# Kernel optimization log

Hardware: AMD Instinct MI355X
Metric: run time of the kernel (lower is better)

## Reference

```python
import jax, jax.numpy as jnp
import numpy as np

D_MODEL = 1024
HEADS = 16
D_K = D_MODEL // HEADS
LN_EPS = 1e-6  # flax nn.LayerNorm default
NEG_INF = -1000000000.0


def _layernorm(x, scale, bias):
    mu = jnp.mean(x, axis=-1, keepdims=True)
    var = jnp.var(x, axis=-1, keepdims=True)
    return (x - mu) * jax.lax.rsqrt(var + LN_EPS) * scale + bias


def setup_inputs() -> dict:
    key = jax.random.key(0)
    ks = jax.random.split(key, 8)
    bs, sq, skv = 4, 2048, 2048
    init = 1.0 / np.sqrt(D_MODEL)  # ~lecun_normal scale for Dense kernels
    return {
        "kv": jax.random.normal(ks[0], (bs, skv, D_MODEL), jnp.float32),
        "q": jax.random.normal(ks[1], (bs, sq, D_MODEL), jnp.float32),
        "mask": jax.random.randint(ks[2], (bs, sq, skv), 0, 2, jnp.int32),
        "Wq": jax.random.normal(ks[3], (D_MODEL, D_MODEL), jnp.float32) * init,
        "bq": jnp.zeros((D_MODEL,), jnp.float32),
        "Wk": jax.random.normal(ks[4], (D_MODEL, D_MODEL), jnp.float32) * init,
        "bk": jnp.zeros((D_MODEL,), jnp.float32),
        "Wv": jax.random.normal(ks[5], (D_MODEL, D_MODEL), jnp.float32) * init,
        "bv": jnp.zeros((D_MODEL,), jnp.float32),
        "qn_scale": jnp.ones((D_MODEL,), jnp.float32),
        "qn_bias": jnp.zeros((D_MODEL,), jnp.float32),
        "kn_scale": jnp.ones((D_MODEL,), jnp.float32),
        "kn_bias": jnp.zeros((D_MODEL,), jnp.float32),
        "vn_scale": jnp.ones((D_MODEL,), jnp.float32),
        "vn_bias": jnp.zeros((D_MODEL,), jnp.float32),
        "Wo": jax.random.normal(ks[6], (D_MODEL, D_MODEL), jnp.float32) * init,
        "bo": jnp.zeros((D_MODEL,), jnp.float32),
    }


def reference(kv, q, mask, Wq, bq, Wk, bk, Wv, bv,
              qn_scale, qn_bias, kn_scale, kn_bias, vn_scale, vn_bias,
              Wo, bo):
    bs = q.shape[0]
    # Dense projections + per-feature LayerNorm on Q/K/V
    query = _layernorm(q @ Wq + bq, qn_scale, qn_bias)
    key = _layernorm(kv @ Wk + bk, kn_scale, kn_bias)
    value = _layernorm(kv @ Wv + bv, vn_scale, vn_bias)
    # [b, s, h, d] -> [b, h, s, d]
    query = query.reshape(bs, -1, HEADS, D_K).transpose(0, 2, 1, 3)
    key = key.reshape(bs, -1, HEADS, D_K).transpose(0, 2, 1, 3)
    value = value.reshape(bs, -1, HEADS, D_K).transpose(0, 2, 1, 3)
    # scores: [b, h, q, k]
    scores = jnp.einsum('bhqd,bhkd->bhqk', query, key) / jnp.sqrt(jnp.asarray(D_K, query.dtype))
    m = mask[:, None, :, :]  # expand_dims(mask, axis=1)
    scores = jnp.where(m == 0, NEG_INF, scores)
    probs = jax.nn.softmax(scores, axis=-1)
    out = jnp.einsum('bhqk,bhkd->bhqd', probs, value)
    out = out.transpose(0, 2, 1, 3).reshape(bs, -1, D_MODEL)
    return out @ Wo + bo
```

## Files before the change

kernel.cpp:

```cpp
#include <hip/hip_runtime.h>
#include <hip/hip_bf16.h>

#define SEQ   2048
#define BS    4
#define DM    1024
#define NH    16
#define ROWS  (BS*SEQ)

using s16x8 = __attribute__((ext_vector_type(8))) short;
using f32x4 = __attribute__((ext_vector_type(4))) float;

#define MFMA16(a,b,c) __builtin_amdgcn_mfma_f32_16x16x32_bf16(a,b,c,0,0,0)

__device__ __forceinline__ short f2bf(float f){
  union { float f; unsigned u; } v; v.f = f;
  unsigned r = (v.u + 0x7FFFu + ((v.u >> 16) & 1u)) >> 16;
  return (short)r;
}

__device__ __forceinline__ float bf2f(short s){
  union { unsigned u; float f; } v; v.u = ((unsigned)(unsigned short)s) << 16;
  return v.f;
}

__device__ __forceinline__ float bpermf(float v, int srcLane){
  union { float f; int i; } u; u.f = v;
  u.i = __builtin_amdgcn_ds_bpermute(srcLane * 4, u.i);
  return u.f;
}

__device__ __forceinline__ void gload_lds16(const void* g, void* l){
  __builtin_amdgcn_global_load_lds(
    (const __attribute__((address_space(1))) unsigned int*)g,
    (__attribute__((address_space(3))) unsigned int*)l, 16, 0, 0);
}

__global__ __launch_bounds__(256) void pack_mask(const int* __restrict__ mask,
                                                 unsigned* __restrict__ bits){
  int t = blockIdx.x * 256 + threadIdx.x;
  unsigned long long b = __ballot(mask[t] != 0);
  int lane = threadIdx.x & 63;
  if (lane == 0)       bits[t >> 5] = (unsigned)b;
  else if (lane == 32) bits[t >> 5] = (unsigned)(b >> 32);
}

__global__ __launch_bounds__(256) void conv_bf16(const float* __restrict__ in,
                                                 short* __restrict__ out){
  int t = blockIdx.x * 256 + threadIdx.x;
  float4 v = ((const float4*)in)[t];
  short4 o;
  o.x = f2bf(v.x); o.y = f2bf(v.y); o.z = f2bf(v.z); o.w = f2bf(v.w);
  ((short4*)out)[t] = o;
}

__global__ __launch_bounds__(256) void transpose_w(const float* __restrict__ W,
                                                   short* __restrict__ Wt){
  __shared__ float tile[32][33];
  int n0 = blockIdx.x * 32, k0 = blockIdx.y * 32;
  int tx = threadIdx.x, ty = threadIdx.y;
  #pragma unroll
  for (int i = 0; i < 32; i += 8)
    tile[ty + i][tx] = W[(size_t)(k0 + ty + i) * DM + n0 + tx];
  __syncthreads();
  #pragma unroll
  for (int i = 0; i < 32; i += 8)
    Wt[(size_t)(n0 + ty + i) * DM + k0 + tx] = f2bf(tile[tx][ty + i]);
}

__global__ __launch_bounds__(256) void gemm_bias(const short* __restrict__ A,
                                                 const short* __restrict__ Bt,
                                                 const float* __restrict__ bias,
                                                 float* __restrict__ C){
  __shared__ short As[128 * 32];
  __shared__ short Bs[128 * 32];
  const int tid = threadIdx.x;
  const int wid = tid >> 6, lane = tid & 63;
  const int m0 = blockIdx.y * 128, n0 = blockIdx.x * 128;
  const int wr = (wid >> 1) * 64, wc = (wid & 1) * 64;
  const int lrow = lane & 15, lk = lane >> 4;
  f32x4 acc[4][4] = {};

  const int e0 = wid * 1024 + lane * 16;
  const int r0 = e0 >> 6, c0 = e0 & 63;
  const int e1 = e0 + 4096;
  const int r1 = e1 >> 6, c1 = e1 & 63;

  const char* Abase = (const char*)A + (size_t)m0 * 2048;
  const char* Bbase = (const char*)Bt + (size_t)n0 * 2048;
  char* AsB = (char*)As;
  char* BsB = (char*)Bs;

  for (int k0 = 0; k0 < DM; k0 += 32) {
    gload_lds16(Abase + (size_t)r0 * 2048 + k0 * 2 + c0, AsB + wid * 1024);
    gload_lds16(Abase + (size_t)r1 * 2048 + k0 * 2 + c1, AsB + 4096 + wid * 1024);
    gload_lds16(Bbase + (size_t)r0 * 2048 + k0 * 2 + c0, BsB + wid * 1024);
    gload_lds16(Bbase + (size_t)r1 * 2048 + k0 * 2 + c1, BsB + 4096 + wid * 1024);
    __syncthreads();
    s16x8 af[4], bf[4];
    #pragma unroll
    for (int mt = 0; mt < 4; mt++)
      af[mt] = *(const s16x8*)(AsB + ((wr + mt * 16 + lrow) * 64 + lk * 16));
    #pragma unroll
    for (int nt = 0; nt < 4; nt++)
      bf[nt] = *(const s16x8*)(BsB + ((wc + nt * 16 + lrow) * 64 + lk * 16));
    #pragma unroll
    for (int mt = 0; mt < 4; mt++)
      #pragma unroll
      for (int nt = 0; nt < 4; nt++)
        acc[mt][nt] = MFMA16(af[mt], bf[nt], acc[mt][nt]);
    __syncthreads();
  }
  #pragma unroll
  for (int nt = 0; nt < 4; nt++) {
    int col = n0 + wc + nt * 16 + lrow;
    float bv = bias[col];
    #pragma unroll
    for (int mt = 0; mt < 4; mt++) {
      #pragma unroll
      for (int r = 0; r < 4; r++) {
        int row = m0 + wr + mt * 16 + lk * 4 + r;
        C[(size_t)row * DM + col] = acc[mt][nt][r] + bv;
      }
    }
  }
}

__global__ __launch_bounds__(256) void ln_to_heads(const float* __restrict__ Y,
                                                   const float* __restrict__ sc,
                                                   const float* __restrict__ bi,
                                                   short* __restrict__ out){
  int row = blockIdx.x;
  int b = row >> 11, s = row & 2047;
  int tid = threadIdx.x;
  float4 v = ((const float4*)(Y + (size_t)row * DM))[tid];
  float sum = v.x + v.y + v.z + v.w;
  float sq  = v.x * v.x + v.y * v.y + v.z * v.z + v.w * v.w;
  #pragma unroll
  for (int o = 32; o; o >>= 1) { sum += __shfl_down(sum, o); sq += __shfl_down(sq, o); }
  __shared__ float red[8];
  int wid = tid >> 6, lane = tid & 63;
  if (!lane) { red[wid] = sum; red[wid + 4] = sq; }
  __syncthreads();
  sum = red[0] + red[1] + red[2] + red[3];
  sq  = red[4] + red[5] + red[6] + red[7];
  float mu = sum * (1.0f / DM);
  float var = sq * (1.0f / DM) - mu * mu;
  float rs = rsqrtf(var + 1e-6f);
  float4 scv = ((const float4*)sc)[tid];
  float4 biv = ((const float4*)bi)[tid];
  short4 o4;
  o4.x = f2bf((v.x - mu) * rs * scv.x + biv.x);
  o4.y = f2bf((v.y - mu) * rs * scv.y + biv.y);
  o4.z = f2bf((v.z - mu) * rs * scv.z + biv.z);
  o4.w = f2bf((v.w - mu) * rs * scv.w + biv.w);
  int c = tid * 4;
  int h = c >> 6, d = c & 63;
  *(short4*)(out + (((size_t)(b * NH + h) * SEQ + s) * 64 + d)) = o4;
}

__global__ __launch_bounds__(256) void transpose_v(const short* __restrict__ Vh,
                                                   short* __restrict__ Vt){
  __shared__ char t[8192];
  const int tid = threadIdx.x;
  const int bh = blockIdx.y;
  const int s0 = blockIdx.x * 64;
  const char* src = (const char*)(Vh + (size_t)bh * SEQ * 64 + (size_t)s0 * 64);
  char* dst = (char*)(Vt + (size_t)bh * 64 * SEQ + s0);
  #pragma unroll
  for (int p = 0; p < 2; p++) {
    int e = p * 4096 + tid * 16;
    int s = e >> 7, d2 = e & 127;
    s16x8 v = *(const s16x8*)(src + (size_t)s * 128 + d2);
    *(s16x8*)(t + s * 128 + (d2 ^ ((s & 7) << 4))) = v;
  }
  __syncthreads();
  #pragma unroll
  for (int p = 0; p < 2; p++) {
    int f = p * 4096 + tid * 16;
    int d = f >> 7;
    int sj = (f & 127) >> 1;
    s16x8 v;
    #pragma unroll
    for (int k = 0; k < 8; k++) {
      int s = sj + k;
      v[k] = *(const short*)(t + s * 128 + ((2 * d) ^ ((s & 7) << 4)));
    }
    *(s16x8*)(dst + (size_t)d * (SEQ * 2) + sj * 2) = v;
  }
}

__global__ __launch_bounds__(256) void attn(const short* __restrict__ Qh,
                                            const short* __restrict__ Kh,
                                            const short* __restrict__ VtG,
                                            const unsigned* __restrict__ mbits,
                                            short* __restrict__ AO){
  __shared__ short Ks[64 * 64];
  __shared__ short Vs[64 * 64];
  __shared__ short Pl[4][16 * 64];
  const int tid = threadIdx.x, wid = tid >> 6, lane = tid & 63;
  const int bh = blockIdx.y, b = bh >> 4, h = bh & 15;
  const int q0 = blockIdx.x * 64;
  const size_t bhoff = (size_t)bh * SEQ * 64;
  const int lrow = lane & 15, lg = lane >> 4;
  const float L2E = 1.44269504f;

  const int qidx = q0 + wid * 16 + lrow;
  s16x8 qf[2];
  {
    const short* qrow = Qh + bhoff + (size_t)qidx * 64 + lg * 8;
    qf[0] = *(const s16x8*)(qrow);
    qf[1] = *(const s16x8*)(qrow + 32);
  }
  f32x4 o[4] = {};
  float m_ = -1e9f, l_ = 0.f;

  const unsigned* mrow = mbits + ((size_t)b * SEQ + qidx) * 64;

  const int e0 = wid * 1024 + lane * 16;
  const int sr0 = e0 >> 7, sc0 = (e0 & 127) ^ ((sr0 & 7) << 4);
  const int e1 = e0 + 4096;
  const int sr1 = e1 >> 7, sc1 = (e1 & 127) ^ ((sr1 & 7) << 4);
  const char* Kbase = (const char*)(Kh + bhoff);
  const char* Vbase = (const char*)(VtG + bhoff);
  char* KsB = (char*)Ks;
  char* VsB = (char*)Vs;
  char* PlB = (char*)&Pl[wid][0];

  for (int k0 = 0; k0 < SEQ; k0 += 64) {
    gload_lds16(Kbase + (size_t)(k0 + sr0) * 128 + sc0, KsB + wid * 1024);
    gload_lds16(Kbase + (size_t)(k0 + sr1) * 128 + sc1, KsB + 4096 + wid * 1024);
    gload_lds16(Vbase + (size_t)sr0 * (SEQ * 2) + k0 * 2 + sc0, VsB + wid * 1024);
    gload_lds16(Vbase + (size_t)sr1 * (SEQ * 2) + k0 * 2 + sc1, VsB + 4096 + wid * 1024);
    __syncthreads();

    const unsigned mw0 = mrow[(k0 >> 5)];
    const unsigned mw1 = mrow[(k0 >> 5) + 1];

    float sv[4][4];
    #pragma unroll
    for (int kt = 0; kt < 4; kt++) {
      f32x4 sacc = {};
      #pragma unroll
      for (int c = 0; c < 2; c++) {
        int krow = kt * 16 + lrow;
        s16x8 kf = *(const s16x8*)(KsB + krow * 128 + ((lg * 16 + 64 * c) ^ ((krow & 7) << 4)));
        sacc = MFMA16(kf, qf[c], sacc);
      }
      unsigned w = (kt < 2) ? mw0 : mw1;
      #pragma unroll
      for (int r = 0; r < 4; r++) {
        int bit = (kt & 1) * 16 + lg * 4 + r;
        bool on = (w >> bit) & 1;
        sv[kt][r] = on ? sacc[r] * 0.125f : -1e9f;
      }
    }
    float t01 = fmaxf(fmaxf(sv[0][0], sv[0][1]), fmaxf(sv[0][2], sv[0][3]));
    float t11 = fmaxf(fmaxf(sv[1][0], sv[1][1]), fmaxf(sv[1][2], sv[1][3]));
    float t21 = fmaxf(fmaxf(sv[2][0], sv[2][1]), fmaxf(sv[2][2], sv[2][3]));
    float t31 = fmaxf(fmaxf(sv[3][0], sv[3][1]), fmaxf(sv[3][2], sv[3][3]));
    float tmax = fmaxf(fmaxf(t01, t11), fmaxf(t21, t31));
    tmax = fmaxf(tmax, __shfl_xor(tmax, 16));
    tmax = fmaxf(tmax, __shfl_xor(tmax, 32));

    if (__any(tmax > m_ + 8.0f)) {
      float mn = fmaxf(m_, tmax);
      float scl = exp2f((m_ - mn) * L2E);
      m_ = mn;
      l_ *= scl;
      #pragma unroll
      for (int r = 0; r < 4; r++) {
        float scr = bpermf(scl, lg * 4 + r);
        o[0][r] *= scr; o[1][r] *= scr; o[2][r] *= scr; o[3][r] *= scr;
      }
    }

    float rsum = 0.f;
    #pragma unroll
    for (int kt = 0; kt < 4; kt++) {
      float ee0 = exp2f((sv[kt][0] - m_) * L2E);
      float ee1 = exp2f((sv[kt][1] - m_) * L2E);
      float ee2 = exp2f((sv[kt][2] - m_) * L2E);
      float ee3 = exp2f((sv[kt][3] - m_) * L2E);
      short b0 = f2bf(ee0), b1 = f2bf(ee1), b2 = f2bf(ee2), b3 = f2bf(ee3);
      rsum += bf2f(b0) + bf2f(b1) + bf2f(b2) + bf2f(b3);
      uint2 wv;
      wv.x = (unsigned)(unsigned short)b0 | ((unsigned)(unsigned short)b1 << 16);
      wv.y = (unsigned)(unsigned short)b2 | ((unsigned)(unsigned short)b3 << 16);
      *(uint2*)(PlB + lrow * 128 + ((32 * kt + 8 * lg) ^ ((lrow & 7) << 4))) = wv;
    }
    rsum += __shfl_xor(rsum, 16);
    rsum += __shfl_xor(rsum, 32);
    l_ += rsum;

    #pragma unroll
    for (int dt = 0; dt < 4; dt++) {
      #pragma unroll
      for (int kc = 0; kc < 2; kc++) {
        s16x8 pf = *(const s16x8*)(PlB + lrow * 128 + ((64 * kc + 16 * lg) ^ ((lrow & 7) << 4)));
        int vrow = dt * 16 + lrow;
        s16x8 vf = *(const s16x8*)(VsB + vrow * 128 + ((64 * kc + 16 * lg) ^ ((vrow & 7) << 4)));
        o[dt] = MFMA16(pf, vf, o[dt]);
      }
    }
    __syncthreads();
  }
  #pragma unroll
  for (int r = 0; r < 4; r++) {
    float lr = bpermf(l_, lg * 4 + r);
    float inv = 1.0f / lr;
    int qrow = q0 + wid * 16 + lg * 4 + r;
    size_t orow = ((size_t)b * SEQ + qrow) * DM + h * 64;
    #pragma unroll
    for (int dt = 0; dt < 4; dt++)
      AO[orow + dt * 16 + lrow] = f2bf(o[dt][r] * inv);
  }
}

extern "C" void kernel_launch(void* const* d_in, const int* in_sizes, int n_in,
                              void* d_out, int out_size, void* d_ws, size_t ws_size,
                              hipStream_t stream) {
  const float* kv  = (const float*)d_in[0];
  const float* q   = (const float*)d_in[1];
  const int*   msk = (const int*)d_in[2];
  const float* Wq  = (const float*)d_in[3];
  const float* bq  = (const float*)d_in[4];
  const float* Wk  = (const float*)d_in[5];
  const float* bk  = (const float*)d_in[6];
  const float* Wv  = (const float*)d_in[7];
  const float* bv  = (const float*)d_in[8];
  const float* qns = (const float*)d_in[9];
  const float* qnb = (const float*)d_in[10];
  const float* kns = (const float*)d_in[11];
  const float* knb = (const float*)d_in[12];
  const float* vns = (const float*)d_in[13];
  const float* vnb = (const float*)d_in[14];
  const float* Wo  = (const float*)d_in[15];
  const float* bo  = (const float*)d_in[16];
  float* out = (float*)d_out;
  char* ws = (char*)d_ws;
  const size_t MB = 1u << 20;

  short* wqt   = (short*)(ws + 0 * MB);
  short* wkt   = (short*)(ws + 2 * MB);
  short* wvt   = (short*)(ws + 4 * MB);
  short* wot   = (short*)(ws + 6 * MB);
  short* qb    = (short*)(ws + 8 * MB);
  short* kvb   = (short*)(ws + 24 * MB);
  float* Y     = (float*)(ws + 40 * MB);
  short* Vt    = (short*)(ws + 40 * MB);
  short* AO    = (short*)(ws + 56 * MB);
  short* Qh    = (short*)(ws + 72 * MB);
  short* Kh    = (short*)(ws + 88 * MB);
  short* Vh    = (short*)(ws + 104 * MB);
  unsigned* mb = (unsigned*)(ws + 120 * MB);

  pack_mask<<<dim3(65536), dim3(256), 0, stream>>>(msk, mb);
  conv_bf16<<<dim3(ROWS * DM / 1024), dim3(256), 0, stream>>>(q, qb);
  conv_bf16<<<dim3(ROWS * DM / 1024), dim3(256), 0, stream>>>(kv, kvb);
  transpose_w<<<dim3(32, 32), dim3(32, 8), 0, stream>>>(Wq, wqt);
  transpose_w<<<dim3(32, 32), dim3(32, 8), 0, stream>>>(Wk, wkt);
  transpose_w<<<dim3(32, 32), dim3(32, 8), 0, stream>>>(Wv, wvt);
  transpose_w<<<dim3(32, 32), dim3(32, 8), 0, stream>>>(Wo, wot);

  gemm_bias<<<dim3(8, 64), dim3(256), 0, stream>>>(qb, wqt, bq, Y);
  ln_to_heads<<<dim3(ROWS), dim3(256), 0, stream>>>(Y, qns, qnb, Qh);
  gemm_bias<<<dim3(8, 64), dim3(256), 0, stream>>>(kvb, wkt, bk, Y);
  ln_to_heads<<<dim3(ROWS), dim3(256), 0, stream>>>(Y, kns, knb, Kh);
  gemm_bias<<<dim3(8, 64), dim3(256), 0, stream>>>(kvb, wvt, bv, Y);
  ln_to_heads<<<dim3(ROWS), dim3(256), 0, stream>>>(Y, vns, vnb, Vh);

  transpose_v<<<dim3(SEQ / 64, BS * NH), dim3(256), 0, stream>>>(Vh, Vt);

  attn<<<dim3(SEQ / 64, BS * NH), dim3(256), 0, stream>>>(Qh, Kh, Vt, mb, AO);

  gemm_bias<<<dim3(8, 64), dim3(256), 0, stream>>>(AO, wot, bo, out);
}
```

Baseline: 567.8 us.

## Process 128 keys per attention iteration, fold softmax scale into Q

```diff
diff --git a/kernel.cpp b/kernel.cpp
--- a/kernel.cpp
+++ b/kernel.cpp
@@ -18,15 +18,16 @@
   return (short)r;
 }
 
-__device__ __forceinline__ float bf2f(short s){
-  union { unsigned u; float f; } v; v.u = ((unsigned)(unsigned short)s) << 16;
-  return v.f;
-}
-
 __device__ __forceinline__ float bpermf(float v, int srcLane){
   union { float f; int i; } u; u.f = v;
   u.i = __builtin_amdgcn_ds_bpermute(srcLane * 4, u.i);
   return u.f;
+}
+
+__device__ __forceinline__ unsigned cvtpk_bf16(float lo, float hi){
+  unsigned r;
+  asm("v_cvt_pk_bf16_f32 %0, %1, %2" : "=v"(r) : "v"(lo), "v"(hi));
+  return r;
 }
 
 __device__ __forceinline__ void gload_lds16(const void* g, void* l){
@@ -128,7 +129,8 @@
 __global__ __launch_bounds__(256) void ln_to_heads(const float* __restrict__ Y,
                                                    const float* __restrict__ sc,
                                                    const float* __restrict__ bi,
-                                                   short* __restrict__ out){
+                                                   short* __restrict__ out,
+                                                   float oscale){
   int row = blockIdx.x;
   int b = row >> 11, s = row & 2047;
   int tid = threadIdx.x;
@@ -149,10 +151,10 @@
   float4 scv = ((const float4*)sc)[tid];
   float4 biv = ((const float4*)bi)[tid];
   short4 o4;
-  o4.x = f2bf((v.x - mu) * rs * scv.x + biv.x);
-  o4.y = f2bf((v.y - mu) * rs * scv.y + biv.y);
-  o4.z = f2bf((v.z - mu) * rs * scv.z + biv.z);
-  o4.w = f2bf((v.w - mu) * rs * scv.w + biv.w);
+  o4.x = f2bf(((v.x - mu) * rs * scv.x + biv.x) * oscale);
+  o4.y = f2bf(((v.y - mu) * rs * scv.y + biv.y) * oscale);
+  o4.z = f2bf(((v.z - mu) * rs * scv.z + biv.z) * oscale);
+  o4.w = f2bf(((v.w - mu) * rs * scv.w + biv.w) * oscale);
   int c = tid * 4;
   int h = c >> 6, d = c & 63;
   *(short4*)(out + (((size_t)(b * NH + h) * SEQ + s) * 64 + d)) = o4;
@@ -194,8 +196,8 @@
                                             const short* __restrict__ VtG,
                                             const unsigned* __restrict__ mbits,
                                             short* __restrict__ AO){
-  __shared__ short Ks[64 * 64];
-  __shared__ short Vs[64 * 64];
+  __shared__ short Ks[2][64 * 64];
+  __shared__ short Vs[2][64 * 64];
   __shared__ short Pl[4][16 * 64];
   const int tid = threadIdx.x, wid = tid >> 6, lane = tid & 63;
   const int bh = blockIdx.y, b = bh >> 4, h = bh & 15;
@@ -214,7 +216,7 @@
   f32x4 o[4] = {};
   float m_ = -1e9f, l_ = 0.f;
 
-  const unsigned* mrow = mbits + ((size_t)b * SEQ + qidx) * 64;
+  const uint4* mrow = (const uint4*)(mbits + ((size_t)b * SEQ + qidx) * 64);
 
   const int e0 = wid * 1024 + lane * 16;
   const int sr0 = e0 >> 7, sc0 = (e0 & 127) ^ ((sr0 & 7) << 4);
@@ -222,48 +224,54 @@
   const int sr1 = e1 >> 7, sc1 = (e1 & 127) ^ ((sr1 & 7) << 4);
   const char* Kbase = (const char*)(Kh + bhoff);
   const char* Vbase = (const char*)(VtG + bhoff);
-  char* KsB = (char*)Ks;
-  char* VsB = (char*)Vs;
+  char* Ks0B = (char*)&Ks[0][0];
+  char* Ks1B = (char*)&Ks[1][0];
+  char* Vs0B = (char*)&Vs[0][0];
+  char* Vs1B = (char*)&Vs[1][0];
   char* PlB = (char*)&Pl[wid][0];
 
-  for (int k0 = 0; k0 < SEQ; k0 += 64) {
-    gload_lds16(Kbase + (size_t)(k0 + sr0) * 128 + sc0, KsB + wid * 1024);
-    gload_lds16(Kbase + (size_t)(k0 + sr1) * 128 + sc1, KsB + 4096 + wid * 1024);
-    gload_lds16(Vbase + (size_t)sr0 * (SEQ * 2) + k0 * 2 + sc0, VsB + wid * 1024);
-    gload_lds16(Vbase + (size_t)sr1 * (SEQ * 2) + k0 * 2 + sc1, VsB + 4096 + wid * 1024);
+  for (int k0 = 0; k0 < SEQ; k0 += 128) {
+    gload_lds16(Kbase + (size_t)(k0 + sr0) * 128 + sc0,      Ks0B + wid * 1024);
+    gload_lds16(Kbase + (size_t)(k0 + sr1) * 128 + sc1,      Ks0B + 4096 + wid * 1024);
+    gload_lds16(Kbase + (size_t)(k0 + 64 + sr0) * 128 + sc0, Ks1B + wid * 1024);
+    gload_lds16(Kbase + (size_t)(k0 + 64 + sr1) * 128 + sc1, Ks1B + 4096 + wid * 1024);
+    gload_lds16(Vbase + (size_t)sr0 * (SEQ * 2) + k0 * 2 + sc0,       Vs0B + wid * 1024);
+    gload_lds16(Vbase + (size_t)sr1 * (SEQ * 2) + k0 * 2 + sc1,       Vs0B + 4096 + wid * 1024);
+    gload_lds16(Vbase + (size_t)sr0 * (SEQ * 2) + k0 * 2 + 128 + sc0, Vs1B + wid * 1024);
+    gload_lds16(Vbase + (size_t)sr1 * (SEQ * 2) + k0 * 2 + 128 + sc1, Vs1B + 4096 + wid * 1024);
+    uint4 mq = mrow[k0 >> 7];
     __syncthreads();
 
-    const unsigned mw0 = mrow[(k0 >> 5)];
-    const unsigned mw1 = mrow[(k0 >> 5) + 1];
-
-    float sv[4][4];
-    #pragma unroll
-    for (int kt = 0; kt < 4; kt++) {
-      f32x4 sacc = {};
-      #pragma unroll
-      for (int c = 0; c < 2; c++) {
-        int krow = kt * 16 + lrow;
-        s16x8 kf = *(const s16x8*)(KsB + krow * 128 + ((lg * 16 + 64 * c) ^ ((krow & 7) << 4)));
-        sacc = MFMA16(kf, qf[c], sacc);
-      }
-      unsigned w = (kt < 2) ? mw0 : mw1;
-      #pragma unroll
-      for (int r = 0; r < 4; r++) {
-        int bit = (kt & 1) * 16 + lg * 4 + r;
-        bool on = (w >> bit) & 1;
-        sv[kt][r] = on ? sacc[r] * 0.125f : -1e9f;
-      }
-    }
-    float t01 = fmaxf(fmaxf(sv[0][0], sv[0][1]), fmaxf(sv[0][2], sv[0][3]));
-    float t11 = fmaxf(fmaxf(sv[1][0], sv[1][1]), fmaxf(sv[1][2], sv[1][3]));
-    float t21 = fmaxf(fmaxf(sv[2][0], sv[2][1]), fmaxf(sv[2][2], sv[2][3]));
-    float t31 = fmaxf(fmaxf(sv[3][0], sv[3][1]), fmaxf(sv[3][2], sv[3][3]));
-    float tmax = fmaxf(fmaxf(t01, t11), fmaxf(t21, t31));
-    tmax = fmaxf(tmax, __shfl_xor(tmax, 16));
-    tmax = fmaxf(tmax, __shfl_xor(tmax, 32));
-
-    if (__any(tmax > m_ + 8.0f)) {
-      float mn = fmaxf(m_, tmax);
+    float sv[8][4];
+    #pragma unroll
+    for (int hf = 0; hf < 2; hf++) {
+      const char* KB = hf ? Ks1B : Ks0B;
+      #pragma unroll
+      for (int kt = 0; kt < 4; kt++) {
+        f32x4 sacc = {};
+        #pragma unroll
+        for (int cc = 0; cc < 2; cc++) {
+          int krow = kt * 16 + lrow;
+          s16x8 kf = *(const s16x8*)(KB + krow * 128 + ((lg * 16 + 64 * cc) ^ ((krow & 7) << 4)));
+          sacc = MFMA16(kf, qf[cc], sacc);
+        }
+        unsigned w = hf ? (kt < 2 ? mq.z : mq.w) : (kt < 2 ? mq.x : mq.y);
+        #pragma unroll
+        for (int r = 0; r < 4; r++) {
+          int bit = (kt & 1) * 16 + lg * 4 + r;
+          sv[hf * 4 + kt][r] = ((w >> bit) & 1) ? sacc[r] : -1e9f;
+        }
+      }
+    }
+    float tm = fmaxf(fmaxf(sv[0][0], sv[0][1]), fmaxf(sv[0][2], sv[0][3]));
+    #pragma unroll
+    for (int c = 1; c < 8; c++)
+      tm = fmaxf(fmaxf(fmaxf(tm, sv[c][0]), fmaxf(sv[c][1], sv[c][2])), sv[c][3]);
+    tm = fmaxf(tm, __shfl_xor(tm, 16));
+    tm = fmaxf(tm, __shfl_xor(tm, 32));
+
+    if (__any(tm > m_ + 8.0f)) {
+      float mn = fmaxf(m_, tm);
       float scl = exp2f((m_ - mn) * L2E);
       m_ = mn;
       l_ *= scl;
@@ -274,34 +282,36 @@
       }
     }
 
+    float mL = m_ * L2E;
     float rsum = 0.f;
     #pragma unroll
-    for (int kt = 0; kt < 4; kt++) {
-      float ee0 = exp2f((sv[kt][0] - m_) * L2E);
-      float ee1 = exp2f((sv[kt][1] - m_) * L2E);
-      float ee2 = exp2f((sv[kt][2] - m_) * L2E);
-      float ee3 = exp2f((sv[kt][3] - m_) * L2E);
-      short b0 = f2bf(ee0), b1 = f2bf(ee1), b2 = f2bf(ee2), b3 = f2bf(ee3);
-      rsum += bf2f(b0) + bf2f(b1) + bf2f(b2) + bf2f(b3);
-      uint2 wv;
-      wv.x = (unsigned)(unsigned short)b0 | ((unsigned)(unsigned short)b1 << 16);
-      wv.y = (unsigned)(unsigned short)b2 | ((unsigned)(unsigned short)b3 << 16);
-      *(uint2*)(PlB + lrow * 128 + ((32 * kt + 8 * lg) ^ ((lrow & 7) << 4))) = wv;
+    for (int hf = 0; hf < 2; hf++) {
+      const char* VB = hf ? Vs1B : Vs0B;
+      #pragma unroll
+      for (int kt = 0; kt < 4; kt++) {
+        int c = hf * 4 + kt;
+        float ee0 = exp2f(sv[c][0] * L2E - mL);
+        float ee1 = exp2f(sv[c][1] * L2E - mL);
+        float ee2 = exp2f(sv[c][2] * L2E - mL);
+        float ee3 = exp2f(sv[c][3] * L2E - mL);
+        rsum += (ee0 + ee1) + (ee2 + ee3);
+        uint2 wv = make_uint2(cvtpk_bf16(ee0, ee1), cvtpk_bf16(ee2, ee3));
+        *(uint2*)(PlB + lrow * 128 + ((32 * kt + 8 * lg) ^ ((lrow & 7) << 4))) = wv;
+      }
+      #pragma unroll
+      for (int dt = 0; dt < 4; dt++) {
+        #pragma unroll
+        for (int kc = 0; kc < 2; kc++) {
+          s16x8 pf = *(const s16x8*)(PlB + lrow * 128 + ((64 * kc + 16 * lg) ^ ((lrow & 7) << 4)));
+          int vrow = dt * 16 + lrow;
+          s16x8 vf = *(const s16x8*)(VB + vrow * 128 + ((64 * kc + 16 * lg) ^ ((vrow & 7) << 4)));
+          o[dt] = MFMA16(pf, vf, o[dt]);
+        }
+      }
     }
     rsum += __shfl_xor(rsum, 16);
     rsum += __shfl_xor(rsum, 32);
     l_ += rsum;
-
-    #pragma unroll
-    for (int dt = 0; dt < 4; dt++) {
-      #pragma unroll
-      for (int kc = 0; kc < 2; kc++) {
-        s16x8 pf = *(const s16x8*)(PlB + lrow * 128 + ((64 * kc + 16 * lg) ^ ((lrow & 7) << 4)));
-        int vrow = dt * 16 + lrow;
-        s16x8 vf = *(const s16x8*)(VsB + vrow * 128 + ((64 * kc + 16 * lg) ^ ((vrow & 7) << 4)));
-        o[dt] = MFMA16(pf, vf, o[dt]);
-      }
-    }
     __syncthreads();
   }
   #pragma unroll
@@ -363,11 +373,11 @@
   transpose_w<<<dim3(32, 32), dim3(32, 8), 0, stream>>>(Wo, wot);
 
   gemm_bias<<<dim3(8, 64), dim3(256), 0, stream>>>(qb, wqt, bq, Y);
-  ln_to_heads<<<dim3(ROWS), dim3(256), 0, stream>>>(Y, qns, qnb, Qh);
+  ln_to_heads<<<dim3(ROWS), dim3(256), 0, stream>>>(Y, qns, qnb, Qh, 0.125f);
   gemm_bias<<<dim3(8, 64), dim3(256), 0, stream>>>(kvb, wkt, bk, Y);
-  ln_to_heads<<<dim3(ROWS), dim3(256), 0, stream>>>(Y, kns, knb, Kh);
+  ln_to_heads<<<dim3(ROWS), dim3(256), 0, stream>>>(Y, kns, knb, Kh, 1.0f);
   gemm_bias<<<dim3(8, 64), dim3(256), 0, stream>>>(kvb, wvt, bv, Y);
-  ln_to_heads<<<dim3(ROWS), dim3(256), 0, stream>>>(Y, vns, vnb, Vh);
+  ln_to_heads<<<dim3(ROWS), dim3(256), 0, stream>>>(Y, vns, vnb, Vh, 1.0f);
 
   transpose_v<<<dim3(SEQ / 64, BS * NH), dim3(256), 0, stream>>>(Vh, Vt);
 
```

Measured after the change: 545.5 us. 3.9% less time.
